# Optimization experiments

Hardware: AMD Instinct MI355X
Metric: run time of the kernel (lower is better)

## Reference

```python
import jax, jax.numpy as jnp
import numpy as np

N_NODES = 50000
N_RELS = 4
E_PER_REL = 400000
D_IN = 256
D_OUT = 256


def setup_inputs() -> dict:
    key = jax.random.key(0)
    k1, k2, k3, k4 = jax.random.split(key, 4)
    x = jax.random.normal(k1, (N_NODES, D_IN), dtype=jnp.float32)
    edges = jax.random.randint(k2, (N_RELS, 2, E_PER_REL), 0, N_NODES, dtype=jnp.int64)
    # xavier-ish scale for weights
    scale = jnp.float32(np.sqrt(2.0 / (D_IN + D_OUT)))
    weight = jax.random.normal(k3, (N_RELS, D_IN, D_OUT), dtype=jnp.float32) * scale
    loop_weight = jax.random.normal(k4, (D_IN, D_OUT), dtype=jnp.float32) * scale
    h_bias = jnp.zeros((D_OUT,), dtype=jnp.float32)
    return {"x": x, "edges": edges, "weight": weight,
            "loop_weight": loop_weight, "h_bias": h_bias}


def reference(x, edges, weight, loop_weight, h_bias):
    """Relational GCN layer: per-relation right-normalized SpMM aggregation,
    summed across relations (HeteroGraphConv default sum), + self-loop matmul,
    + bias, + tanh. Dropout rate is 0.0 (identity)."""
    num_nodes = x.shape[0]
    n_rels = edges.shape[0]
    agg = jnp.zeros((num_nodes, weight.shape[-1]), dtype=x.dtype)
    ones_e = jnp.ones((edges.shape[-1],), dtype=x.dtype)
    for r in range(n_rels):  # small fixed loop over relation types
        src, dst = edges[r, 0], edges[r, 1]
        # aggregate source features into destinations (sum), then right-normalize
        msg = jax.ops.segment_sum(x[src], dst, num_segments=num_nodes)  # [N, D_IN]
        deg = jax.ops.segment_sum(ones_e, dst, num_segments=num_nodes)
        deg = jnp.maximum(deg, 1.0)  # DGL clamps zero in-degrees to 1
        h_r = (msg / deg[:, None]) @ weight[r]  # [N, D_OUT]
        agg = agg + h_r
    h = agg + x @ loop_weight + h_bias
    return jnp.tanh(h)
```

## Files before the change

kernel.cpp:

```cpp
#include <hip/hip_runtime.h>
#include <cstdint>
#include <cstddef>

constexpr int N = 50000;
constexpr int D = 256;
constexpr int E = 400000;
constexpr int R = 4;
constexpr int AROWS = 50048;
constexpr int MTILES = AROWS / 64;
constexpr int KCAT = 1280;
constexpr int NT = KCAT / 32;


constexpr int NBPR = 196;
constexpr int NBKT = NBPR * R;
constexpr int BCAP = 2560;
constexpr int MAXDEG = 32;
constexpr int ECHUNK = 2048;
constexpr int NCHUNKS = (E + ECHUNK - 1) / ECHUNK;
constexpr int MAXOVF = 4096;

constexpr int PART_BLOCKS = NCHUNKS * R;
constexpr int CONV_BLOCKS = (AROWS * 32 + 255) / 256;
constexpr int WT_BLOCKS = (2 * 40 * 4 * 128 + 255) / 256;
constexpr int PREP_BLOCKS = PART_BLOCKS + CONV_BLOCKS + WT_BLOCKS;

typedef _Float16 f16x8 __attribute__((ext_vector_type(8)));
typedef float f32x4 __attribute__((ext_vector_type(4)));

__device__ __forceinline__ void load_lds16(const void* g, void* l) {
    __builtin_amdgcn_global_load_lds(
        (const __attribute__((address_space(1))) void*)g,
        (__attribute__((address_space(3))) void*)l, 16, 0, 0);
}

__device__ __forceinline__ float fast_tanh(float x) {
    const float xc = fminf(fmaxf(x, -9.0f), 9.0f);
    const float t = __builtin_amdgcn_exp2f(xc * 2.8853900817779268f);
    return (t - 1.0f) / (t + 1.0f);
}

__global__ __launch_bounds__(256)
void prep_kernel(const float* __restrict__ x, const int* __restrict__ edges,
                 const float* __restrict__ w, const float* __restrict__ lw,
                 _Float16* __restrict__ xh, _Float16* __restrict__ wt,
                 int* __restrict__ gcnt, uint* __restrict__ buckets,
                 int* __restrict__ ovf_n, int2* __restrict__ ovf) {
    __shared__ int hist[256], base[256], run[256], gbase[256], ps[256];
    __shared__ int tot_s;
    __shared__ uint staging[ECHUNK];

    const int bid = blockIdx.x;
    const int t = threadIdx.x;

    if (bid < PART_BLOCKS) {
        const int chunk = bid >> 2;
        const int r = bid & 3;
        const int* srcp = edges + (size_t)r * 2 * E;
        const int* dstp = srcp + E;
        const int e0 = chunk * ECHUNK;

        hist[t] = 0;
        run[t] = 0;
        __syncthreads();

        uint rec[8];
#pragma unroll
        for (int u = 0; u < 8; ++u) {
            const int i = e0 + u * 256 + t;
            if (i < E) {
                rec[u] = ((uint)srcp[i] << 16) | (uint)dstp[i];
                atomicAdd(&hist[(rec[u] & 0xFFFFu) >> 8], 1);
            } else {
                rec[u] = 0xFFFFFFFFu;
            }
        }
        __syncthreads();

        const int v = hist[t];
        ps[t] = v;
        __syncthreads();
        for (int off = 1; off < 256; off <<= 1) {
            const int xx = (t >= off) ? ps[t - off] : 0;
            __syncthreads();
            ps[t] += xx;
            __syncthreads();
        }
        base[t] = ps[t] - v;
        if (t == 255) tot_s = ps[255];
        if (v > 0) gbase[t] = atomicAdd(&gcnt[r * NBPR + t], v);
        __syncthreads();

#pragma unroll
        for (int u = 0; u < 8; ++u) {
            if (rec[u] != 0xFFFFFFFFu) {
                const int bl = (rec[u] & 0xFFFFu) >> 8;
                const int pos = base[bl] + atomicAdd(&run[bl], 1);
                staging[pos] = rec[u];
            }
        }
        __syncthreads();

        const int total = tot_s;
        for (int j = t; j < total; j += 256) {
            const uint rc = staging[j];
            const int bl = (rc & 0xFFFFu) >> 8;
            const int gp = gbase[bl] + (j - base[bl]);
            if (gp < BCAP) {
                buckets[(size_t)(r * NBPR + bl) * BCAP + gp] = rc;
            } else {
                const int o = atomicAdd(ovf_n, 1);
                if (o < MAXOVF)
                    ovf[o] = make_int2(r * N + (int)(rc & 0xFFFFu), (int)(rc >> 16));
            }
        }
    } else if (bid < PART_BLOCKS + CONV_BLOCKS) {
        const long i = (long)(bid - PART_BLOCKS) * 256 + t;
        if (i >= (long)AROWS * 32) return;
        const int n = (int)(i >> 5);
        const int cx = (int)(i & 31);
        f16x8 vv;
        if (n < N) {
            const float4* s =
                reinterpret_cast<const float4*>(x + (size_t)n * D + cx * 8);
            const float4 a = s[0], b = s[1];
            vv[0] = (_Float16)a.x; vv[1] = (_Float16)a.y;
            vv[2] = (_Float16)a.z; vv[3] = (_Float16)a.w;
            vv[4] = (_Float16)b.x; vv[5] = (_Float16)b.y;
            vv[6] = (_Float16)b.z; vv[7] = (_Float16)b.w;
        } else {
#pragma unroll
            for (int j = 0; j < 8; ++j) vv[j] = (_Float16)0.f;
        }
        *reinterpret_cast<f16x8*>(xh + (size_t)n * D + cx * 8) = vv;
    } else {
        const int i = (bid - PART_BLOCKS - CONV_BLOCKS) * 256 + t;
        if (i >= 2 * 40 * 4 * 128) return;
        const int nt = i / 20480;
        const int r1 = i - nt * 20480;
        const int kt = r1 >> 9;
        const int r2 = r1 & 511;
        const int pl = r2 >> 7;
        const int row = r2 & 127;
        const int kb = kt * 32 + pl * 8;
        const int col = nt * 128 + row;
        f16x8 vv;
#pragma unroll
        for (int j = 0; j < 8; ++j) {
            const int k = kb + j;
            const float val = (k < 1024)
                                  ? w[((k >> 8) << 16) + ((k & 255) << 8) + col]
                                  : lw[((k - 1024) << 8) + col];
            vv[j] = (_Float16)val;
        }
        *reinterpret_cast<f16x8*>(wt + (size_t)i * 8) = vv;
    }
}

__global__ __launch_bounds__(256)
void bucket_gather_kernel(const uint* __restrict__ buckets,
                          const int* __restrict__ gcnt,
                          const _Float16* __restrict__ xh,
                          const int2* __restrict__ ovf,
                          const int* __restrict__ ovf_n,
                          _Float16* __restrict__ A_t) {
    __shared__ int lcnt[32];
    __shared__ ushort lslots[32][MAXDEG];
    __shared__ _Float16 msg[32][264];
    const int t = threadIdx.x;
    const int b = blockIdx.x % NBKT;
    const int part = blockIdx.x / NBKT;
    const int r = b / NBPR;
    const int bl = b - r * NBPR;
    const int d0 = (bl << 8) + (part << 5);
    if (d0 >= N) return;
    const int mt = d0 >> 6;
    const int rowoff = d0 & 63;

    if (t < 32) lcnt[t] = 0;
    __syncthreads();

    const int nb = min(gcnt[b], BCAP);
    const uint* brec = buckets + (size_t)b * BCAP;
    for (int j = t; j < nb; j += 256) {
        const uint rc = brec[j];
        const int wi = (int)(rc & 0xFFFFu) - d0;
        if ((unsigned)wi < 32u) {
            const int pos = atomicAdd(&lcnt[wi], 1);
            if (pos < MAXDEG) lslots[wi][pos] = (ushort)(rc >> 16);
        }
    }
    __syncthreads();

    const int lane = t & 63;
    const int wv = t >> 6;
    const int hf = lane >> 5;
    const int cx = lane & 31;
    const int on = min(*ovf_n, MAXOVF);

    auto xrow = [&](int s) -> f16x8 {
        return *reinterpret_cast<const f16x8*>(xh + (size_t)s * D + cx * 8);
    };

    for (int wi = wv * 8; wi < wv * 8 + 8; ++wi) {
        const int d = d0 + wi;
        const int m = (d < N) ? lcnt[wi] : 0;
        float acc[8] = {};
        if (m <= MAXDEG) {
            int j = hf;
            for (; j + 6 < m; j += 8) {
                const int s0 = lslots[wi][j];
                const int s1 = lslots[wi][j + 2];
                const int s2 = lslots[wi][j + 4];
                const int s3 = lslots[wi][j + 6];
                const f16x8 v0 = xrow(s0);
                const f16x8 v1 = xrow(s1);
                const f16x8 v2 = xrow(s2);
                const f16x8 v3 = xrow(s3);
#pragma unroll
                for (int k = 0; k < 8; ++k)
                    acc[k] += ((float)v0[k] + (float)v1[k]) +
                              ((float)v2[k] + (float)v3[k]);
            }
            for (; j < m; j += 2) {
                const f16x8 vv = xrow(lslots[wi][j]);
#pragma unroll
                for (int k = 0; k < 8; ++k) acc[k] += (float)vv[k];
            }
        } else {
            for (int j = hf; j < nb; j += 2) {
                const uint rc = brec[j];
                if ((int)(rc & 0xFFFFu) == d) {
                    const f16x8 vv = xrow((int)(rc >> 16));
#pragma unroll
                    for (int k = 0; k < 8; ++k) acc[k] += (float)vv[k];
                }
            }
        }
        int ecnt = m;
        if (on > 0 && d < N) {
            const int wfull = r * N + d;
            for (int o = 0; o < on; ++o) {
                const int2 e2 = ovf[o];
                if (e2.x == wfull) {
                    ecnt++;
                    if (hf == 0) {
                        const f16x8 vv = xrow(e2.y);
#pragma unroll
                        for (int k = 0; k < 8; ++k) acc[k] += (float)vv[k];
                    }
                }
            }
        }
#pragma unroll
        for (int k = 0; k < 8; ++k) acc[k] += __shfl_xor(acc[k], 32);
        if (hf == 0) {
            const float rs = 1.0f / fmaxf((float)ecnt, 1.0f);
            f16x8 o8;
#pragma unroll
            for (int k = 0; k < 8; ++k) o8[k] = (_Float16)(acc[k] * rs);
            *reinterpret_cast<f16x8*>(&msg[wi][cx * 8]) = o8;
        }
    }
    __syncthreads();

    _Float16* dst = A_t + ((size_t)mt * 32 + r * 8) * 2048 + (size_t)rowoff * 8;
#pragma unroll
    for (int i = 0; i < 4; ++i) {
        const int g = i * 256 + t;
        const int row = g & 31;
        const int q = g >> 5;
        const int c = (q >> 2) * 32 + (q & 3) * 8;
        const f16x8 v = *reinterpret_cast<const f16x8*>(&msg[row][c]);
        *reinterpret_cast<f16x8*>(dst + (size_t)q * 512 + (size_t)row * 8) = v;
    }
}

__global__ __launch_bounds__(256)
void gemm_final_kernel(const _Float16* __restrict__ A_t,
                       const _Float16* __restrict__ xh,
                       const _Float16* __restrict__ WT_t,
                       const float* __restrict__ bias, float* __restrict__ C) {
    __shared__ _Float16 As[3][4][64][8];
    __shared__ _Float16 Bs[3][4][128][8];

    const int t = threadIdx.x;
    const int lane = t & 63;
    const int w = t >> 6;
    const int nt = blockIdx.x;
    const int mt = blockIdx.y;
    const long m0 = (long)mt * 64;

    f32x4 acc[8];
#pragma unroll
    for (int j = 0; j < 8; ++j) acc[j] = (f32x4){0.f, 0.f, 0.f, 0.f};

    const int kg = lane >> 4;
    const int rr = lane & 15;

    auto stage = [&](int kt, int buf) {
        const _Float16* asrc =
            (kt < 32)
                ? A_t + ((size_t)mt * 32 + kt) * 2048 + w * 512 + lane * 8
                : xh + (size_t)(m0 + lane) * D + (kt - 32) * 32 + w * 8;
        load_lds16(asrc, &As[buf][0][0][0] + w * 512);
        const _Float16* bsrc = WT_t + ((size_t)nt * 40 + kt) * 4096 + w * 1024 + lane * 8;
        load_lds16(bsrc, &Bs[buf][0][0][0] + w * 1024);
        load_lds16(bsrc + 512, &Bs[buf][0][0][0] + w * 1024 + 512);
    };

    auto compute = [&](int buf) {
        f16x8 af, bf[8];
        af = *reinterpret_cast<const f16x8*>(&As[buf][kg][w * 16 + rr][0]);
#pragma unroll
        for (int g = 0; g < 8; ++g)
            bf[g] = *reinterpret_cast<const f16x8*>(&Bs[buf][kg][g * 16 + rr][0]);
        __builtin_amdgcn_s_setprio(1);
#pragma unroll
        for (int j = 0; j < 8; ++j)
            acc[j] = __builtin_amdgcn_mfma_f32_16x16x32_f16(af, bf[j], acc[j], 0, 0, 0);
        __builtin_amdgcn_s_setprio(0);
    };

    stage(0, 0);
    stage(1, 1);

    for (int kt = 0; kt < NT - 2; ++kt) {
        asm volatile("s_waitcnt vmcnt(3)" ::: "memory");
        __builtin_amdgcn_sched_barrier(0);
        __builtin_amdgcn_s_barrier();
        __builtin_amdgcn_sched_barrier(0);
        stage(kt + 2, (kt + 2) % 3);
        compute(kt % 3);
    }
    asm volatile("s_waitcnt vmcnt(3)" ::: "memory");
    __builtin_amdgcn_sched_barrier(0);
    __builtin_amdgcn_s_barrier();
    __builtin_amdgcn_sched_barrier(0);
    compute((NT - 2) % 3);
    asm volatile("s_waitcnt vmcnt(0)" ::: "memory");
    __builtin_amdgcn_sched_barrier(0);
    __builtin_amdgcn_s_barrier();
    __builtin_amdgcn_sched_barrier(0);
    compute((NT - 1) % 3);

    const int crow0 = (lane >> 4) * 4;
    const int ccol = lane & 15;
    const long rowb = m0 + w * 16 + crow0;
#pragma unroll
    for (int j = 0; j < 8; ++j) {
        const int col = nt * 128 + j * 16 + ccol;
        const float b = bias[col];
#pragma unroll
        for (int q = 0; q < 4; ++q) {
            const long rgl = rowb + q;
            if (rgl < N) C[rgl * 256 + col] = fast_tanh(acc[j][q] + b);
        }
    }
}

extern "C" void kernel_launch(void* const* d_in, const int* in_sizes, int n_in,
                              void* d_out, int out_size, void* d_ws, size_t ws_size,
                              hipStream_t stream) {
    const float* x           = (const float*)d_in[0];
    const int*   edges       = (const int*)d_in[1];
    const float* weight      = (const float*)d_in[2];
    const float* loop_weight = (const float*)d_in[3];
    const float* h_bias      = (const float*)d_in[4];
    float*       out         = (float*)d_out;
    (void)in_sizes; (void)n_in; (void)out_size; (void)ws_size;

    size_t off = 0;
    auto carve = [&](size_t bytes) -> void* {
        void* p = (char*)d_ws + off;
        off = (off + bytes + 255) & ~(size_t)255;
        return p;
    };

    _Float16* A_t  = (_Float16*)carve((size_t)MTILES * 32 * 2048 * sizeof(_Float16));
    _Float16* xh   = (_Float16*)carve((size_t)AROWS * D * sizeof(_Float16));
    _Float16* WT_t = (_Float16*)carve((size_t)2 * 40 * 4096 * sizeof(_Float16));
    int*      gcnt  = (int*)carve((size_t)NBKT * sizeof(int) + 256);
    int*      ovf_n = gcnt + NBKT;
    int2*     ovf   = (int2*)carve((size_t)MAXOVF * sizeof(int2));
    uint* buckets = (uint*)d_out;

    hipMemsetAsync(gcnt, 0, (size_t)NBKT * sizeof(int) + 256, stream);

    prep_kernel<<<PREP_BLOCKS, 256, 0, stream>>>(x, edges, weight, loop_weight,
                                                 xh, WT_t, gcnt, buckets,
                                                 ovf_n, ovf);

    bucket_gather_kernel<<<NBKT * 8, 256, 0, stream>>>(buckets, gcnt, xh,
                                                       ovf, ovf_n, A_t);
    gemm_final_kernel<<<dim3(2, MTILES), 256, 0, stream>>>(A_t, xh, WT_t, h_bias, out);
}
```

Measured before the change: 221.7 us.

## Store self-loop x tiles in GEMM-tiled layout and use wave-shuffle scan

When workspace allows, the prep kernel also writes the fp16 x rows into the tiled A_t buffer (k-tiles 32..39), so the GEMM reads all 40 k-tiles from one contiguous tiled layout instead of strided xh rows. The histogram prefix sum is also replaced by a wave-level shuffle scan plus a tiny cross-wave combine, removing many block barriers. This costs extra workspace and an additional write of x-sized data in prep.

```diff
diff --git a/kernel.cpp b/kernel.cpp
--- a/kernel.cpp
+++ b/kernel.cpp
@@ -44,9 +44,10 @@
 void prep_kernel(const float* __restrict__ x, const int* __restrict__ edges,
                  const float* __restrict__ w, const float* __restrict__ lw,
                  _Float16* __restrict__ xh, _Float16* __restrict__ wt,
+                 _Float16* __restrict__ A_t, int ktA,
                  int* __restrict__ gcnt, uint* __restrict__ buckets,
                  int* __restrict__ ovf_n, int2* __restrict__ ovf) {
-    __shared__ int hist[256], base[256], run[256], gbase[256], ps[256];
+    __shared__ int hist[256], base[256], run[256], gbase[256], ps[80];
     __shared__ int tot_s;
     __shared__ uint staging[ECHUNK];
 
@@ -78,16 +79,28 @@
         __syncthreads();
 
         const int v = hist[t];
-        ps[t] = v;
-        __syncthreads();
-        for (int off = 1; off < 256; off <<= 1) {
-            const int xx = (t >= off) ? ps[t - off] : 0;
-            __syncthreads();
-            ps[t] += xx;
-            __syncthreads();
-        }
-        base[t] = ps[t] - v;
-        if (t == 255) tot_s = ps[255];
+        const int lane = t & 63;
+        int sc = v;
+#pragma unroll
+        for (int off = 1; off < 64; off <<= 1) {
+            const int y = __shfl_up(sc, off);
+            if (lane >= off) sc += y;
+        }
+        if (lane == 63) ps[64 + (t >> 6)] = sc;
+        __syncthreads();
+        if (t == 0) {
+            int run0 = 0;
+#pragma unroll
+            for (int wv2 = 0; wv2 < 4; ++wv2) {
+                const int s2 = ps[64 + wv2];
+                ps[68 + wv2] = run0;
+                run0 += s2;
+            }
+        }
+        __syncthreads();
+        const int incl = sc + ps[68 + (t >> 6)];
+        base[t] = incl - v;
+        if (t == 255) tot_s = incl;
         if (v > 0) gbase[t] = atomicAdd(&gcnt[r * NBPR + t], v);
         __syncthreads();
 
@@ -133,6 +146,13 @@
             for (int j = 0; j < 8; ++j) vv[j] = (_Float16)0.f;
         }
         *reinterpret_cast<f16x8*>(xh + (size_t)n * D + cx * 8) = vv;
+        if (ktA == 40) {
+            const int mt2 = n >> 6;
+            const size_t toff =
+                (((size_t)mt2 * 40 + 32 + (cx >> 2)) * 4 + (cx & 3)) * 512 +
+                (size_t)(n & 63) * 8;
+            *reinterpret_cast<f16x8*>(A_t + toff) = vv;
+        }
     } else {
         const int i = (bid - PART_BLOCKS - CONV_BLOCKS) * 256 + t;
         if (i >= 2 * 40 * 4 * 128) return;
@@ -163,7 +183,7 @@
                           const _Float16* __restrict__ xh,
                           const int2* __restrict__ ovf,
                           const int* __restrict__ ovf_n,
-                          _Float16* __restrict__ A_t) {
+                          _Float16* __restrict__ A_t, int ktA) {
     __shared__ int lcnt[32];
     __shared__ ushort lslots[32][MAXDEG];
     __shared__ _Float16 msg[32][264];
@@ -264,7 +284,8 @@
     }
     __syncthreads();
 
-    _Float16* dst = A_t + ((size_t)mt * 32 + r * 8) * 2048 + (size_t)rowoff * 8;
+    _Float16* dst =
+        A_t + ((size_t)mt * ktA + r * 8) * 2048 + (size_t)rowoff * 8;
 #pragma unroll
     for (int i = 0; i < 4; ++i) {
         const int g = i * 256 + t;
@@ -279,7 +300,7 @@
 __global__ __launch_bounds__(256)
 void gemm_final_kernel(const _Float16* __restrict__ A_t,
                        const _Float16* __restrict__ xh,
-                       const _Float16* __restrict__ WT_t,
+                       const _Float16* __restrict__ WT_t, int ktA,
                        const float* __restrict__ bias, float* __restrict__ C) {
     __shared__ _Float16 As[3][4][64][8];
     __shared__ _Float16 Bs[3][4][128][8];
@@ -300,8 +321,8 @@
 
     auto stage = [&](int kt, int buf) {
         const _Float16* asrc =
-            (kt < 32)
-                ? A_t + ((size_t)mt * 32 + kt) * 2048 + w * 512 + lane * 8
+            (kt < ktA)
+                ? A_t + ((size_t)mt * ktA + kt) * 2048 + w * 512 + lane * 8
                 : xh + (size_t)(m0 + lane) * D + (kt - 32) * 32 + w * 8;
         load_lds16(asrc, &As[buf][0][0][0] + w * 512);
         const _Float16* bsrc = WT_t + ((size_t)nt * 40 + kt) * 4096 + w * 1024 + lane * 8;
@@ -368,7 +389,14 @@
     const float* loop_weight = (const float*)d_in[3];
     const float* h_bias      = (const float*)d_in[4];
     float*       out         = (float*)d_out;
-    (void)in_sizes; (void)n_in; (void)out_size; (void)ws_size;
+    (void)in_sizes; (void)n_in; (void)out_size;
+
+    const size_t fixed = (size_t)AROWS * D * 2
+                       + (size_t)2 * 40 * 4096 * 2
+                       + (size_t)NBKT * 4 + 256
+                       + (size_t)MAXOVF * 8 + 4096;
+    const int ktA =
+        (ws_size >= (size_t)MTILES * 40 * 2048 * 2 + fixed) ? 40 : 32;
 
     size_t off = 0;
     auto carve = [&](size_t bytes) -> void* {
@@ -377,7 +405,7 @@
         return p;
     };
 
-    _Float16* A_t  = (_Float16*)carve((size_t)MTILES * 32 * 2048 * sizeof(_Float16));
+    _Float16* A_t  = (_Float16*)carve((size_t)MTILES * ktA * 2048 * sizeof(_Float16));
     _Float16* xh   = (_Float16*)carve((size_t)AROWS * D * sizeof(_Float16));
     _Float16* WT_t = (_Float16*)carve((size_t)2 * 40 * 4096 * sizeof(_Float16));
     int*      gcnt  = (int*)carve((size_t)NBKT * sizeof(int) + 256);
@@ -388,10 +416,11 @@
     hipMemsetAsync(gcnt, 0, (size_t)NBKT * sizeof(int) + 256, stream);
 
     prep_kernel<<<PREP_BLOCKS, 256, 0, stream>>>(x, edges, weight, loop_weight,
-                                                 xh, WT_t, gcnt, buckets,
-                                                 ovf_n, ovf);
+                                                 xh, WT_t, A_t, ktA, gcnt,
+                                                 buckets, ovf_n, ovf);
 
     bucket_gather_kernel<<<NBKT * 8, 256, 0, stream>>>(buckets, gcnt, xh,
-                                                       ovf, ovf_n, A_t);
-    gemm_final_kernel<<<dim3(2, MTILES), 256, 0, stream>>>(A_t, xh, WT_t, h_bias, out);
-}
+                                                       ovf, ovf_n, A_t, ktA);
+    gemm_final_kernel<<<dim3(2, MTILES), 256, 0, stream>>>(A_t, xh, WT_t, ktA,
+                                                           h_bias, out);
+}
```

Result: slower. 230.0 us (+3.8%).
